# Performance work log

Hardware: AMD Instinct MI355X
Metric: run time of the kernel (lower is better)

The kernel has to match this reference:

```python
import jax, jax.numpy as jnp
import numpy as np

D_MODEL = 512; D_STATE = 64; D_CONV = 4; EXPAND = 1; HEADDIM = 128; NGROUPS = 2; CHUNK = 256
D_INNER = EXPAND * (D_MODEL // 2)          # 256
NHEADS = D_INNER // HEADDIM                 # 2
CONV_DIM = D_INNER + 2 * NGROUPS * D_STATE  # 512
D_IN_PROJ = CONV_DIM + NHEADS               # 514

def silu(x):
    return x * jax.nn.sigmoid(x)

def conv1x1(x, w, b):
    # x: (b,c,h,w), w: (o,c)
    return jnp.einsum('bchw,oc->bohw', x, w) + b[None, :, None, None]

def dwconv3x3(x, w, b):
    # depthwise 3x3, SAME padding; w: (c,1,3,3)
    c = x.shape[1]
    y = jax.lax.conv_general_dilated(x, w, (1, 1), 'SAME', feature_group_count=c,
                                     dimension_numbers=('NCHW', 'OIHW', 'NCHW'))
    return y + b[None, :, None, None]

def causal_dwconv1d(x, w, b):
    # x: (b,L,c); w: (c,k). Torch pads k-1 both sides then slices [:L] -> causal left pad.
    k = w.shape[1]
    xp = jnp.pad(x, ((0, 0), (k - 1, 0), (0, 0))).transpose(0, 2, 1)  # (b,c,L+k-1)
    y = jax.lax.conv_general_dilated(xp, w[:, None, :], (1,), 'VALID',
                                     feature_group_count=w.shape[0],
                                     dimension_numbers=('NCH', 'OIH', 'NCH'))
    return y.transpose(0, 2, 1) + b

def axis_attn(x, qw, qb, fw, fb, axis):
    # DualAxisAggAttn single-axis step
    qkv = conv1x1(x, qw, qb)
    c = x.shape[1]
    q, k, v = qkv[:, :1], qkv[:, 1:1 + c], qkv[:, 1 + c:]
    dim = -1 if axis == 'W' else -2
    scores = jax.nn.softmax(q, axis=dim)
    ctx = jnp.sum(k * scores, axis=dim, keepdims=True)
    out = x + jax.nn.sigmoid(v) * ctx
    return conv1x1(out, fw, fb)

def segsum(x):
    # x: (...,T) -> (...,T,T) lower-triangular segment sums, -inf above diagonal
    T = x.shape[-1]
    cs = jnp.cumsum(x, -1)
    d = cs[..., :, None] - cs[..., None, :]
    mask = jnp.tril(jnp.ones((T, T), bool))
    return jnp.where(mask, d, -jnp.inf)

def ssd(X, A, B, C, chunk):
    # Mamba2 SSD chunked scan. X: (b,l,h,p) = x*dt; A: (b,l,h) = dt*A_head; B,C: (b,l,h,n)
    b, l, h, p = X.shape; n = B.shape[-1]; c = l // chunk
    X = X.reshape(b, c, chunk, h, p)
    B = B.reshape(b, c, chunk, h, n)
    C = C.reshape(b, c, chunk, h, n)
    A = A.reshape(b, c, chunk, h).transpose(0, 3, 1, 2)  # (b,h,c,L)
    Acs = jnp.cumsum(A, -1)
    L = jnp.exp(segsum(A))  # (b,h,c,L,L) intra-chunk decay
    Yd = jnp.einsum('bclhn,bcshn,bhcls,bcshp->bclhp', C, B, L, X)
    dec = jnp.exp(Acs[..., -1:] - Acs)
    st = jnp.einsum('bclhn,bhcl,bclhp->bchpn', B, dec, X)  # chunk end-states
    st = jnp.concatenate([jnp.zeros_like(st[:, :1]), st], 1)
    dchunk = jnp.exp(segsum(jnp.pad(Acs[..., -1], ((0, 0), (0, 0), (1, 0)))))
    st = jnp.einsum('bhzc,bchpn->bzhpn', dchunk, st)[:, :-1]  # states entering each chunk
    Yo = jnp.einsum('bclhn,bchpn,bhcl->bclhp', C, st, jnp.exp(Acs))
    return (Yd + Yo).reshape(b, l, h, p)

def setup_inputs() -> dict:
    key = jax.random.key(0)
    ks = jax.random.split(key, 12)
    s = 0.02
    p = {}
    p['u'] = jax.random.normal(ks[0], (8, D_MODEL, 64, 64), jnp.float32)
    p['sc_w1'] = jax.random.normal(ks[1], (D_MODEL, D_MODEL)) * s
    p['sc_b1'] = jnp.zeros((D_MODEL,))
    p['sc_wdw'] = jax.random.normal(ks[2], (D_MODEL, 1, 3, 3)) * s
    p['sc_bdw'] = jnp.zeros((D_MODEL,))
    p['sc_w2'] = jax.random.normal(ks[3], (D_INNER, D_MODEL)) * s
    p['sc_b2'] = jnp.zeros((D_INNER,))
    p['mc_w'] = jax.random.normal(ks[4], (D_INNER, D_MODEL)) * s
    p['mc_b'] = jnp.zeros((D_INNER,))
    p['qkvW_w'] = jax.random.normal(ks[5], (1 + 2 * D_INNER, D_INNER)) * s
    p['qkvW_b'] = jnp.zeros((1 + 2 * D_INNER,))
    p['qkvH_w'] = jax.random.normal(ks[6], (1 + 2 * D_INNER, D_INNER)) * s
    p['qkvH_b'] = jnp.zeros((1 + 2 * D_INNER,))
    p['fuseW_w'] = jax.random.normal(ks[7], (D_INNER, D_INNER)) * s
    p['fuseW_b'] = jnp.zeros((D_INNER,))
    p['fuseH_w'] = jax.random.normal(ks[8], (D_INNER, D_INNER)) * s
    p['fuseH_b'] = jnp.zeros((D_INNER,))
    p['in_proj_w'] = jax.random.normal(ks[9], (D_IN_PROJ, D_INNER)) * s
    p['conv1d_w'] = jax.random.normal(ks[10], (CONV_DIM, D_CONV)) * s
    p['conv1d_b'] = jnp.zeros((CONV_DIM,))
    dt = np.exp(np.linspace(np.log(1e-3), np.log(0.1), NHEADS))
    p['dt_bias'] = jnp.asarray(dt + np.log(-np.expm1(-dt)), jnp.float32)
    p['A_log'] = jnp.asarray(np.log(np.linspace(1.0, 16.0, NHEADS)), jnp.float32)
    p['D'] = jnp.ones((NHEADS,))
    p['norm_w'] = jnp.ones((D_INNER,))
    p['outp_w'] = jax.random.normal(ks[11], (D_MODEL, 2 * D_INNER)) * s
    p['outp_b'] = jnp.zeros((D_MODEL,))
    return p

def reference(u, sc_w1, sc_b1, sc_wdw, sc_bdw, sc_w2, sc_b2, mc_w, mc_b,
              qkvW_w, qkvW_b, qkvH_w, qkvH_b, fuseW_w, fuseW_b, fuseH_w, fuseH_b,
              in_proj_w, conv1d_w, conv1d_b, dt_bias, A_log, D, norm_w, outp_w, outp_b):
    b, _, H, W = u.shape
    # short_conv branch (light_ConvBlock: 1x1 -> dw3x3 -> 1x1, all SiLU; BN folded into bias)
    z = silu(conv1x1(u, sc_w1, sc_b1))
    z = silu(dwconv3x3(z, sc_wdw, sc_bdw))
    z = silu(conv1x1(z, sc_w2, sc_b2))
    # main branch
    x = silu(conv1x1(u, mc_w, mc_b))
    x = axis_attn(x, qkvW_w, qkvW_b, fuseW_w, fuseW_b, 'W')
    x = axis_attn(x, qkvH_w, qkvH_b, fuseH_w, fuseH_b, 'H')
    seqlen = H * W
    u2 = x.transpose(0, 2, 3, 1).reshape(b, seqlen, D_INNER)  # b (h w) c
    xbcdt = u2 @ in_proj_w.T  # (b,l,d_in_proj)
    xBC = xbcdt[..., :CONV_DIM]
    dt = jax.nn.softplus(xbcdt[..., CONV_DIM:] + dt_bias)  # (b,l,h)
    A = -jnp.exp(A_log)  # (h,)
    xBC = silu(causal_dwconv1d(xBC, conv1d_w, conv1d_b))
    xs = xBC[..., :D_INNER]
    Bs = xBC[..., D_INNER:D_INNER + NGROUPS * D_STATE].reshape(b, seqlen, NGROUPS, D_STATE)
    Cs = xBC[..., D_INNER + NGROUPS * D_STATE:].reshape(b, seqlen, NGROUPS, D_STATE)
    Xh = xs.reshape(b, seqlen, NHEADS, HEADDIM)
    rep = NHEADS // NGROUPS
    Bh = jnp.repeat(Bs, rep, axis=2)
    Ch = jnp.repeat(Cs, rep, axis=2)
    y = ssd(Xh * dt[..., None], dt * A[None, None, :], Bh, Ch, CHUNK)
    y = y + Xh * D[None, None, :, None]  # D skip connection
    y = y.reshape(b, seqlen, D_INNER)
    # RMSNormGated with z=None -> plain RMSNorm
    y = y * jax.lax.rsqrt(jnp.mean(y * y, -1, keepdims=True) + 1e-5) * norm_w
    y = y.reshape(b, H, W, D_INNER).transpose(0, 3, 1, 2)
    y = jnp.concatenate([z, y], axis=1)
    return conv1x1(y, outp_w, outp_b)
```

## Files before the change

kernel.cpp:

```cpp
#include <hip/hip_runtime.h>
#include <hip/hip_bf16.h>
#include <cstddef>
#include <cstdint>

#define PTOT 32768
#define HWSZ 4096

typedef __attribute__((ext_vector_type(8))) short bf16x8;
typedef __attribute__((ext_vector_type(4))) short s16x4;
typedef __attribute__((ext_vector_type(4))) float f32x4;

__device__ __forceinline__ float sigf(float x){ return 1.f/(1.f+__expf(-x)); }
__device__ __forceinline__ float siluf(float x){ return x*sigf(x); }
__device__ __forceinline__ short f2b(float x){
  __hip_bfloat16 h = __float2bfloat16(x);
  return *reinterpret_cast<short*>(&h);
}
__device__ __forceinline__ float b2f(short s){
  unsigned u = ((unsigned)(unsigned short)s) << 16;
  return __uint_as_float(u);
}

__device__ __forceinline__ void gload16(const void* g, void* l){
  __builtin_amdgcn_global_load_lds(
      (const __attribute__((address_space(1))) unsigned int*)g,
      (__attribute__((address_space(3))) unsigned int*)l, 16, 0, 0);
}

__global__ __launch_bounds__(256) void k_cvtw(
    const float* __restrict__ s0, const float* __restrict__ s1, const float* __restrict__ s2,
    const float* __restrict__ s3, const float* __restrict__ s4,
    short* __restrict__ dst){
  int idx = blockIdx.x*256 + threadIdx.x;
  const float* s; int off;
  if      (idx <  262144){ s=s0; off=idx; }
  else if (idx <  393216){ s=s1; off=idx- 262144; }
  else if (idx <  524288){ s=s2; off=idx- 393216; }
  else if (idx <  655616){ s=s3; off=idx- 524288; }
  else if (idx <  917760){ s=s4; off=idx- 655616; }
  else return;
  dst[idx] = f2b(s[off]);
}

__global__ __launch_bounds__(256) void k_wcomp(
    const float* __restrict__ qkvHw, const float* __restrict__ fuWw,
    const float* __restrict__ fuWb,  const float* __restrict__ qkvHb,
    const float* __restrict__ inpw,  const float* __restrict__ fuHw,
    const float* __restrict__ fuHb,
    const float* __restrict__ scb1,  const float* __restrict__ mcb,
    short* __restrict__ wcomb, float* __restrict__ bcomb,
    short* __restrict__ wi2,   float* __restrict__ bi2,
    float* __restrict__ bzx)
{
  int blk = blockIdx.x;
  int tid = threadIdx.x;
  __shared__ float as[256];
  __shared__ float red[256];
  if (blk < 513){
    int i = blk;
    int r = (i==512) ? 0 : (i+1);
    as[tid]  = qkvHw[(size_t)r*256 + tid];
    red[tid] = as[tid] * fuWb[tid];
    __syncthreads();
    for (int off=128; off; off>>=1){ if (tid<off) red[tid]+=red[tid+off]; __syncthreads(); }
    float acc = 0.f;
    #pragma unroll 8
    for (int k=0;k<256;k++) acc += as[k]*fuWw[(size_t)k*256 + tid];
    wcomb[(size_t)(256+i)*256 + tid] = f2b(acc);
    if (tid==0) bcomb[256+i] = red[0] + qkvHb[r];
  } else if (blk < 769){
    int j = blk - 513;
    wcomb[(size_t)j*256 + tid] = f2b(fuWw[(size_t)j*256 + tid]);
    if (tid==0) bcomb[j] = fuWb[j];
  } else if (blk < 1283){
    int j = blk - 769;
    as[tid]  = inpw[(size_t)j*256 + tid];
    red[tid] = as[tid] * fuHb[tid];
    __syncthreads();
    for (int off=128; off; off>>=1){ if (tid<off) red[tid]+=red[tid+off]; __syncthreads(); }
    float acc = 0.f;
    #pragma unroll 8
    for (int k=0;k<256;k++) acc += as[k]*fuHw[(size_t)k*256 + tid];
    wi2[(size_t)j*256 + tid] = f2b(acc);
    if (tid==0) bi2[j] = red[0];
  } else {
    int j = (blk - 1283)*256 + tid;
    bzx[j] = (j < 512) ? scb1[j] : mcb[j-512];
  }
}

__global__ __launch_bounds__(256) void k_transpose(const float* __restrict__ in, short* __restrict__ out){
  __shared__ float tile[64][33];
  int b = blockIdx.z;
  int c0 = blockIdx.y * 64;
  int s0 = blockIdx.x * 32;
  int tx = threadIdx.x, ty = threadIdx.y;
  const float* ip = in + ((size_t)b*512 + c0)*HWSZ + s0;
  for (int i = ty; i < 64; i += 8) tile[i][tx] = ip[(size_t)i*HWSZ + tx];
  __syncthreads();
  for (int i = ty; i < 32; i += 8){
    unsigned lo = (unsigned)(unsigned short)f2b(tile[2*tx][i]);
    unsigned hi = (unsigned)(unsigned short)f2b(tile[2*tx+1][i]);
    unsigned pk = lo | (hi<<16);
    *reinterpret_cast<unsigned*>(&out[((size_t)((b<<12) + s0 + i))*512 + c0 + 2*tx]) = pk;
  }
}

template<int ACT, int OUT_NCHW>
__global__ __launch_bounds__(256) void k_gemm(
    const short* __restrict__ A0, const short* __restrict__ A1,
    int kSplit, int lda0, int lda1,
    const short* __restrict__ Wt, const float* __restrict__ bias,
    void* __restrict__ Cpv, int N, int K, int ldc, int qkvPerm,
    short* __restrict__ Cp2, int nSplit2, int ldc2)
{
  __shared__ short Alds[3][128*32];
  __shared__ short Wlds[2][128*32];

  int tid = threadIdx.x;
  int lane = tid & 63;
  int wv = tid >> 6;
  int wr = wv >> 1, wc = wv & 1;
  int lr = lane & 15, lh = lane >> 4;
  int bm = blockIdx.x * 128;
  int bn = blockIdx.y * 128;

  int rl = lane >> 2;
  int kg = (lane & 3) << 3;

  int ar[2], wnr[2];
  #pragma unroll
  for (int j=0;j<2;j++){
    int r = wv*32 + j*16 + rl;
    ar[j] = bm + r;
    int n = bn + r; if (n > N-1) n = N-1;
    wnr[j] = qkvPerm ? ((n==512)?0:(n+1)) : n;
  }

  auto stage_a = [&](int buf, int t){
    int k0 = t << 5;
    #pragma unroll
    for (int j=0;j<2;j++){
      const short* asrc;
      if (k0 < kSplit) asrc = A0 + (size_t)ar[j]*lda0 + (k0 + kg);
      else             asrc = A1 + (size_t)ar[j]*lda1 + (k0 - kSplit + kg);
      gload16(asrc, &Alds[buf][(wv*32 + j*16)*32]);
    }
  };
  auto stage_w = [&](int buf, int t){
    int k0 = t << 5;
    #pragma unroll
    for (int j=0;j<2;j++){
      const short* bsrc = Wt + (size_t)wnr[j]*K + (k0 + kg);
      gload16(bsrc, &Wlds[buf][(wv*32 + j*16)*32]);
    }
  };

  f32x4 acc[4][4];
  #pragma unroll
  for (int i=0;i<4;i++)
    #pragma unroll
    for (int j=0;j<4;j++) acc[i][j] = (f32x4){0.f,0.f,0.f,0.f};

  int NT = K >> 5;
  stage_w(0, 0);
  __builtin_amdgcn_sched_barrier(0);
  stage_a(0, 0);
  __builtin_amdgcn_sched_barrier(0);
  stage_a(1, 1);
  for (int t=0; t<NT; t++){
    int ab = t % 3, wb = t & 1;
    if (t+1 < NT) asm volatile("s_waitcnt vmcnt(2)" ::: "memory");
    else          asm volatile("s_waitcnt vmcnt(0)" ::: "memory");
    __builtin_amdgcn_s_barrier();
    __builtin_amdgcn_sched_barrier(0);
    if (t+1 < NT) stage_w(wb^1, t+1);
    __builtin_amdgcn_sched_barrier(0);
    if (t+2 < NT) stage_a((t+2)%3, t+2);
    __builtin_amdgcn_sched_barrier(0);
    bf16x8 af[4], bfr[4];
    #pragma unroll
    for (int mi=0;mi<4;mi++)
      af[mi] = *reinterpret_cast<const bf16x8*>(&Alds[ab][(wr*64 + mi*16 + lr)*32 + lh*8]);
    #pragma unroll
    for (int ni=0;ni<4;ni++)
      bfr[ni] = *reinterpret_cast<const bf16x8*>(&Wlds[wb][(wc*64 + ni*16 + lr)*32 + lh*8]);
    #pragma unroll
    for (int mi=0;mi<4;mi++)
      #pragma unroll
      for (int ni=0;ni<4;ni++)
        acc[mi][ni] = __builtin_amdgcn_mfma_f32_16x16x32_bf16(af[mi], bfr[ni], acc[mi][ni], 0, 0, 0);
  }

  if (!OUT_NCHW){
    short* Cp = (short*)Cpv;
    #pragma unroll
    for (int mi=0;mi<4;mi++){
      int m = bm + wr*64 + mi*16 + lh*4;
      #pragma unroll
      for (int ni=0;ni<4;ni++){
        int n = bn + wc*64 + ni*16 + lr;
        if (n < N){
          int wn = qkvPerm ? ((n==512)?0:(n+1)) : n;
          float bb = bias ? bias[wn] : 0.f;
          #pragma unroll
          for (int r=0;r<4;r++){
            float v = acc[mi][ni][r] + bb;
            if (ACT==1) v = siluf(v);
            short sv = f2b(v);
            if (n < nSplit2) Cp[(size_t)(m+r)*ldc + n] = sv;
            else             Cp2[(size_t)(m+r)*ldc2 + (n - nSplit2)] = sv;
          }
        }
      }
    }
  } else {
    float* Cp = (float*)Cpv;
    float* Sep = ((float*)Alds) + wv*16*68;
    #pragma unroll
    for (int mi=0;mi<4;mi++){
      __syncthreads();
      #pragma unroll
      for (int ni=0;ni<4;ni++){
        int n = bn + wc*64 + ni*16 + lr;
        float bb = (bias && n < N) ? bias[n] : 0.f;
        #pragma unroll
        for (int r=0;r<4;r++){
          float v = acc[mi][ni][r] + bb;
          if (ACT==1) v = siluf(v);
          Sep[(lh*4+r)*68 + ni*16 + lr] = v;
        }
      }
      __syncthreads();
      int m = bm + wr*64 + mi*16 + lr;
      size_t mb = ((size_t)(m>>12)*ldc)*HWSZ + (m & 4095);
      #pragma unroll
      for (int g=0; g<16; g++){
        int nl = g*4 + lh;
        float v = Sep[lr*68 + nl];
        int nn = bn + wc*64 + nl;
        if (nn < N) Cp[mb + (size_t)nn*HWSZ] = v;
      }
    }
  }
}

__global__ __launch_bounds__(256) void k_dwconv3x3(const short* __restrict__ in,
    const float* __restrict__ w, const float* __restrict__ bias, short* __restrict__ out){
  int tid = threadIdx.x;
  int cq = tid & 127;
  int wi = tid >> 7;
  int bw = blockIdx.x;
  int b  = bw >> 5;
  int wc = ((bw & 31) << 1) | wi;
  int h0 = blockIdx.y << 4;
  int c  = cq << 2;

  float arr[36];
  {
    const float* wp = &w[c*9];
    #pragma unroll
    for (int t=0;t<9;t++){
      f32x4 v = *reinterpret_cast<const f32x4*>(wp + t*4);
      arr[t*4+0]=v[0]; arr[t*4+1]=v[1]; arr[t*4+2]=v[2]; arr[t*4+3]=v[3];
    }
  }
  f32x4 bias4 = *reinterpret_cast<const f32x4*>(&bias[c]);

  int pb = b << 12;
  auto ldrow = [&](int r, int dw)->f32x4 {
    int ww = wc + dw;
    if ((unsigned)r >= 64u || (unsigned)ww >= 64u) return (f32x4){0.f,0.f,0.f,0.f};
    s16x4 v = *reinterpret_cast<const s16x4*>(&in[((size_t)(pb + (r<<6) + ww) << 9) + c]);
    return (f32x4){b2f(v[0]), b2f(v[1]), b2f(v[2]), b2f(v[3])};
  };

  f32x4 a00,a01,a02,a10,a11,a12,a20,a21,a22;
  a00=ldrow(h0-1,-1); a01=ldrow(h0-1,0); a02=ldrow(h0-1,1);
  a10=ldrow(h0  ,-1); a11=ldrow(h0  ,0); a12=ldrow(h0  ,1);
  #pragma unroll
  for (int hh=0; hh<16; hh++){
    int h = h0 + hh;
    a20=ldrow(h+1,-1); a21=ldrow(h+1,0); a22=ldrow(h+1,1);
    s16x4 o;
    #pragma unroll
    for (int j=0;j<4;j++){
      float v = bias4[j];
      v = fmaf(a00[j], arr[j*9+0], v);
      v = fmaf(a01[j], arr[j*9+1], v);
      v = fmaf(a02[j], arr[j*9+2], v);
      v = fmaf(a10[j], arr[j*9+3], v);
      v = fmaf(a11[j], arr[j*9+4], v);
      v = fmaf(a12[j], arr[j*9+5], v);
      v = fmaf(a20[j], arr[j*9+6], v);
      v = fmaf(a21[j], arr[j*9+7], v);
      v = fmaf(a22[j], arr[j*9+8], v);
      o[j] = f2b(siluf(v));
    }
    *reinterpret_cast<s16x4*>(&out[((size_t)(pb + (h<<6) + wc) << 9) + c]) = o;
    a00=a10; a01=a11; a02=a12;
    a10=a20; a11=a21; a12=a22;
  }
}

__global__ __launch_bounds__(256) void k_attn(const short* __restrict__ x, int xld,
    const short* __restrict__ qkv, int qld, short* __restrict__ out, int axisH){
  int bl = blockIdx.x;
  int b = bl >> 6, line = bl & 63;
  __shared__ float es[64];
  __shared__ float qs[64];
  int tid = threadIdx.x;
  int pbase = b << 12;
  if (tid < 64){
    int p = axisH ? (pbase | (tid<<6) | line) : (pbase | (line<<6) | tid);
    qs[tid] = b2f(qkv[(size_t)p*qld + 512]);
  }
  __syncthreads();
  float mx = -1e30f;
  for (int t=0;t<64;t++) mx = fmaxf(mx, qs[t]);
  if (tid < 64) es[tid] = __expf(qs[tid]-mx);
  __syncthreads();
  float s = 0.f;
  for (int t=0;t<64;t++) s += es[t];
  float inv = 1.f/s;
  int c = tid;
  float ctx = 0.f;
  for (int t=0;t<64;t++){
    int p = axisH ? (pbase | (t<<6) | line) : (pbase | (line<<6) | t);
    ctx += es[t]*b2f(qkv[(size_t)p*qld + c]);
  }
  ctx *= inv;
  for (int t=0;t<64;t++){
    int p = axisH ? (pbase | (t<<6) | line) : (pbase | (line<<6) | t);
    float vv = b2f(qkv[(size_t)p*qld + 256 + c]);
    float xv = b2f(x[(size_t)p*xld + c]);
    out[(size_t)p*256 + c] = f2b(xv + sigf(vv)*ctx);
  }
}

__global__ __launch_bounds__(256) void k_dt(const short* __restrict__ xbcdt,
    const float* __restrict__ dt_bias, float* __restrict__ dtb){
  int idx = blockIdx.x*256 + threadIdx.x;
  if (idx >= PTOT*2) return;
  int p = idx >> 1, h = idx & 1;
  float xv = b2f(xbcdt[(size_t)p*520 + 512 + h]) + dt_bias[h];
  float sp = (xv > 20.f) ? xv : log1pf(__expf(xv));
  dtb[idx] = sp;
}

__global__ __launch_bounds__(256) void k_conv1d(const short* __restrict__ xbcdt,
    const float* __restrict__ w, const float* __restrict__ bias, short* __restrict__ xBC){
  int tid = threadIdx.x;
  int cq = tid & 127;
  int c  = cq << 2;
  int half = tid >> 7;
  int bs = blockIdx.x;
  int b  = bs >> 7;
  int t0 = ((((bs & 127) << 1) | half) << 4);

  float wk[16];
  {
    const float* wp = &w[c*4];
    #pragma unroll
    for (int t=0;t<4;t++){
      f32x4 v = *reinterpret_cast<const f32x4*>(wp + t*4);
      wk[t*4+0]=v[0]; wk[t*4+1]=v[1]; wk[t*4+2]=v[2]; wk[t*4+3]=v[3];
    }
  }
  f32x4 bias4 = *reinterpret_cast<const f32x4*>(&bias[c]);

  int pb = b << 12;
  auto ld = [&](int t)->f32x4 {
    if (t < 0) return (f32x4){0.f,0.f,0.f,0.f};
    s16x4 v = *reinterpret_cast<const s16x4*>(&xbcdt[(size_t)(pb + t)*520 + c]);
    return (f32x4){b2f(v[0]), b2f(v[1]), b2f(v[2]), b2f(v[3])};
  };

  f32x4 x0,x1,x2,x3;
  x0 = ld(t0-3); x1 = ld(t0-2); x2 = ld(t0-1);
  #pragma unroll
  for (int tt=0; tt<16; tt++){
    int t = t0 + tt;
    x3 = ld(t);
    s16x4 o;
    #pragma unroll
    for (int j=0;j<4;j++){
      float v = bias4[j];
      v = fmaf(x0[j], wk[j*4+0], v);
      v = fmaf(x1[j], wk[j*4+1], v);
      v = fmaf(x2[j], wk[j*4+2], v);
      v = fmaf(x3[j], wk[j*4+3], v);
      o[j] = f2b(siluf(v));
    }
    *reinterpret_cast<s16x4*>(&xBC[((size_t)(pb + t) << 9) + c]) = o;
    x0=x1; x1=x2; x2=x3;
  }
}

__global__ __launch_bounds__(256) void k_ssd_states(
  const short* __restrict__ xBC, const float* __restrict__ dtb, const float* __restrict__ A_log,
  float* __restrict__ states, float* __restrict__ AcsG, float* __restrict__ AtotG)
{
  int ci = blockIdx.x, h = blockIdx.y, b = blockIdx.z;
  int tid = threadIdx.x;
  __shared__ float sa[256], sb[256];
  __shared__ float Bs[64][65];
  __shared__ float Xs[64][136];
  int base = (b<<12) | (ci<<8);
  float Ah = -__expf(A_log[h]);
  sa[tid] = dtb[(size_t)(base + tid)*2 + h] * Ah;
  __syncthreads();
  float* src = sa; float* dst = sb;
  for (int off=1; off<256; off<<=1){
    float v = src[tid];
    if (tid >= off) v += src[tid - off];
    dst[tid] = v;
    __syncthreads();
    float* tswap = src; src = dst; dst = tswap;
  }
  float acs = src[tid];
  float atot = src[255];
  AcsG[((size_t)((b*2+h)*16 + ci))*256 + tid] = acs;
  if (tid == 0) AtotG[(b*2+h)*16 + ci] = atot;

  int tn = tid >> 4;
  int tp = tid & 15;
  float acc[4][8];
  #pragma unroll
  for (int i=0;i<4;i++)
    #pragma unroll
    for (int j=0;j<8;j++) acc[i][j]=0.f;

  for (int t0=0; t0<256; t0+=64){
    __syncthreads();
    for (int e = tid; e < 64*64; e += 256){
      int t = e >> 6, n = e & 63;
      float d = __expf(atot - src[t0 + t]);
      Bs[t][n] = b2f(xBC[(size_t)(base + t0 + t)*512 + 256 + (h<<6) + n]) * d;
    }
    for (int e = tid; e < 64*128; e += 256){
      int t = e >> 7, pp = e & 127;
      Xs[t][pp] = b2f(xBC[(size_t)(base + t0 + t)*512 + (h<<7) + pp]) * dtb[(size_t)(base + t0 + t)*2 + h];
    }
    __syncthreads();
    for (int t=0;t<64;t++){
      float bv[4], xv[8];
      #pragma unroll
      for (int i=0;i<4;i++) bv[i]=Bs[t][tn*4+i];
      #pragma unroll
      for (int j=0;j<8;j++) xv[j]=Xs[t][tp*8+j];
      #pragma unroll
      for (int i=0;i<4;i++)
        #pragma unroll
        for (int j=0;j<8;j++) acc[i][j] = fmaf(bv[i], xv[j], acc[i][j]);
    }
  }
  float* stp = states + (((size_t)(b*16+ci)*2 + h) << 13);
  #pragma unroll
  for (int i=0;i<4;i++){
    float4 s0 = {acc[i][0], acc[i][1], acc[i][2], acc[i][3]};
    float4 s1 = {acc[i][4], acc[i][5], acc[i][6], acc[i][7]};
    float* pdst = &stp[(tn*4+i)*128 + tp*8];
    *reinterpret_cast<float4*>(pdst)   = s0;
    *reinterpret_cast<float4*>(pdst+4) = s1;
  }
}

__global__ __launch_bounds__(256) void k_ssd_scan(const float* __restrict__ states,
    const float* __restrict__ AtotG, float* __restrict__ R){
  int bh = blockIdx.x;
  int b = bh >> 1, h = bh & 1;
  int tid = threadIdx.x;
  float r[32];
  #pragma unroll
  for (int j=0;j<32;j++) r[j]=0.f;
  for (int ci=0; ci<16; ci++){
    size_t off = (((size_t)(b*16+ci)*2) + h) << 13;
    #pragma unroll
    for (int j=0;j<32;j++) R[off + tid + (j<<8)] = r[j];
    if (ci < 15){
      float sc = __expf(AtotG[bh*16 + ci]);
      #pragma unroll
      for (int j=0;j<32;j++) r[j] = fmaf(sc, r[j], states[off + tid + (j<<8)]);
    }
  }
}

__global__ __launch_bounds__(256) void k_ssd_y(
  const short* __restrict__ xBC, const float* __restrict__ dtb,
  const float* __restrict__ AcsG, const float* __restrict__ R,
  const float* __restrict__ Dp, float* __restrict__ yraw)
{
  int bx = blockIdx.x;
  int ci = bx >> 2, lt = bx & 3;
  int h = blockIdx.y, b = blockIdx.z;
  int tid = threadIdx.x, lane = tid & 63, w = tid >> 6;
  int lg = lane >> 4, lr = lane & 15;
  int base = (b<<12) | (ci<<8);
  int l0 = lt << 6;

  __shared__ short Cbf[64*72];
  __shared__ short Bbf[64*72];
  __shared__ short Xt [128*76];
  __shared__ short Sbf[64*72];
  __shared__ float acs_l[64], acs_s[64], dt_s[64];

  const float* acsrow = AcsG + ((size_t)((b*2+h)*16 + ci))*256;

  {
    int row = tid >> 2, c0 = (tid & 3) << 4;
    const short* src = &xBC[(size_t)(base + l0 + row)*512 + 384 + (h<<6) + c0];
    *reinterpret_cast<bf16x8*>(&Cbf[row*72 + c0])     = *reinterpret_cast<const bf16x8*>(src);
    *reinterpret_cast<bf16x8*>(&Cbf[row*72 + c0 + 8]) = *reinterpret_cast<const bf16x8*>(src+8);
  }
  if (tid < 64) acs_l[tid] = acsrow[l0 + tid];

  f32x4 yacc[8];
  #pragma unroll
  for (int pf=0;pf<8;pf++) yacc[pf] = (f32x4){0.f,0.f,0.f,0.f};

  for (int s0 = 0; s0 <= l0; s0 += 64){
    __syncthreads();
    {
      int row = tid >> 2, c0 = (tid & 3) << 4;
      const short* src = &xBC[(size_t)(base + s0 + row)*512 + 256 + (h<<6) + c0];
      *reinterpret_cast<bf16x8*>(&Bbf[row*72 + c0])     = *reinterpret_cast<const bf16x8*>(src);
      *reinterpret_cast<bf16x8*>(&Bbf[row*72 + c0 + 8]) = *reinterpret_cast<const bf16x8*>(src+8);
    }
    {
      int s = tid >> 2;
      int p0 = (tid & 3) << 5;
      const short* src = &xBC[(size_t)(base + s0 + s)*512 + (h<<7) + p0];
      #pragma unroll
      for (int q=0;q<4;q++){
        bf16x8 v = *reinterpret_cast<const bf16x8*>(src + q*8);
        #pragma unroll
        for (int e=0;e<8;e++) Xt[(p0 + q*8 + e)*76 + s] = v[e];
      }
    }
    if (tid < 64){
      acs_s[tid] = acsrow[s0 + tid];
      dt_s[tid]  = dtb[(size_t)(base + s0 + tid)*2 + h];
    }
    __syncthreads();

    f32x4 sacc[4];
    #pragma unroll
    for (int f=0;f<4;f++) sacc[f] = (f32x4){0.f,0.f,0.f,0.f};
    bf16x8 ca0 = *reinterpret_cast<const bf16x8*>(&Cbf[(w*16+lr)*72 + lg*8]);
    bf16x8 ca1 = *reinterpret_cast<const bf16x8*>(&Cbf[(w*16+lr)*72 + 32 + lg*8]);
    #pragma unroll
    for (int f=0;f<4;f++){
      bf16x8 bb0 = *reinterpret_cast<const bf16x8*>(&Bbf[(f*16+lr)*72 + lg*8]);
      bf16x8 bb1 = *reinterpret_cast<const bf16x8*>(&Bbf[(f*16+lr)*72 + 32 + lg*8]);
      sacc[f] = __builtin_amdgcn_mfma_f32_16x16x32_bf16(ca0, bb0, sacc[f], 0, 0, 0);
      sacc[f] = __builtin_amdgcn_mfma_f32_16x16x32_bf16(ca1, bb1, sacc[f], 0, 0, 0);
    }
    #pragma unroll
    for (int f=0;f<4;f++){
      #pragma unroll
      for (int r=0;r<4;r++){
        int ll = w*16 + lg*4 + r;
        int ss = f*16 + lr;
        float v = 0.f;
        if (s0 + ss <= l0 + ll)
          v = sacc[f][r] * __expf(acs_l[ll] - acs_s[ss]) * dt_s[ss];
        Sbf[ll*72 + ss] = f2b(v);
      }
    }
    __syncthreads();

    bf16x8 sa0 = *reinterpret_cast<const bf16x8*>(&Sbf[(w*16+lr)*72 + lg*8]);
    bf16x8 sa1 = *reinterpret_cast<const bf16x8*>(&Sbf[(w*16+lr)*72 + 32 + lg*8]);
    #pragma unroll
    for (int pf=0;pf<8;pf++){
      bf16x8 x0 = *reinterpret_cast<const bf16x8*>(&Xt[(pf*16+lr)*76 + lg*8]);
      bf16x8 x1 = *reinterpret_cast<const bf16x8*>(&Xt[(pf*16+lr)*76 + 32 + lg*8]);
      yacc[pf] = __builtin_amdgcn_mfma_f32_16x16x32_bf16(sa0, x0, yacc[pf], 0, 0, 0);
      yacc[pf] = __builtin_amdgcn_mfma_f32_16x16x32_bf16(sa1, x1, yacc[pf], 0, 0, 0);
    }
  }

  __syncthreads();
  {
    size_t roff = (((size_t)(b*16+ci)*2) + h) << 13;
    int n = tid >> 2;
    const float* src = R + roff + (size_t)n*128;
    #pragma unroll
    for (int j=0;j<8;j++){
      int p = ((tid & 3) << 2) + (j << 4);
      float4 f = *reinterpret_cast<const float4*>(&src[p]);
      Xt[(p+0)*76 + n] = f2b(f.x);
      Xt[(p+1)*76 + n] = f2b(f.y);
      Xt[(p+2)*76 + n] = f2b(f.z);
      Xt[(p+3)*76 + n] = f2b(f.w);
    }
  }
  __syncthreads();
  f32x4 racc[8];
  #pragma unroll
  for (int pf=0;pf<8;pf++) racc[pf] = (f32x4){0.f,0.f,0.f,0.f};
  {
    bf16x8 ca0 = *reinterpret_cast<const bf16x8*>(&Cbf[(w*16+lr)*72 + lg*8]);
    bf16x8 ca1 = *reinterpret_cast<const bf16x8*>(&Cbf[(w*16+lr)*72 + 32 + lg*8]);
    #pragma unroll
    for (int pf=0;pf<8;pf++){
      bf16x8 x0 = *reinterpret_cast<const bf16x8*>(&Xt[(pf*16+lr)*76 + lg*8]);
      bf16x8 x1 = *reinterpret_cast<const bf16x8*>(&Xt[(pf*16+lr)*76 + 32 + lg*8]);
      racc[pf] = __builtin_amdgcn_mfma_f32_16x16x32_bf16(ca0, x0, racc[pf], 0, 0, 0);
      racc[pf] = __builtin_amdgcn_mfma_f32_16x16x32_bf16(ca1, x1, racc[pf], 0, 0, 0);
    }
  }

  float Dh = Dp[h];
  float el[4];
  #pragma unroll
  for (int r=0;r<4;r++) el[r] = __expf(acs_l[w*16 + lg*4 + r]);
  #pragma unroll
  for (int pf=0;pf<8;pf++){
    #pragma unroll
    for (int r=0;r<4;r++){
      int ll = w*16 + lg*4 + r;
      int p = pf*16 + lr;
      size_t pix = (size_t)(base + l0 + ll);
      float xraw = b2f(xBC[pix*512 + (h<<7) + p]);
      yraw[pix*256 + (h<<7) + p] = yacc[pf][r] + el[r]*racc[pf][r] + Dh*xraw;
    }
  }
}

__global__ __launch_bounds__(256) void k_rmsnorm(const float* __restrict__ yraw,
    const float* __restrict__ nw, short* __restrict__ ynorm){
  int p = blockIdx.x;
  int tid = threadIdx.x;
  float v = yraw[(size_t)p*256 + tid];
  float sq = v*v;
  for (int off=32; off; off>>=1) sq += __shfl_down(sq, off);
  __shared__ float wsum[4];
  if ((tid & 63) == 0) wsum[tid>>6] = sq;
  __syncthreads();
  float tot = wsum[0]+wsum[1]+wsum[2]+wsum[3];
  float scale = rsqrtf(tot*(1.f/256.f) + 1e-5f);
  ynorm[(size_t)p*256 + tid] = f2b(v*scale*nw[tid]);
}

extern "C" void kernel_launch(void* const* d_in, const int* in_sizes, int n_in,
                              void* d_out, int out_size, void* d_ws, size_t ws_size,
                              hipStream_t stream)
{
  (void)in_sizes; (void)n_in; (void)out_size; (void)ws_size;
  const float* u        = (const float*)d_in[0];
  const float* sc_w1    = (const float*)d_in[1];
  const float* sc_b1    = (const float*)d_in[2];
  const float* sc_wdw   = (const float*)d_in[3];
  const float* sc_bdw   = (const float*)d_in[4];
  const float* sc_w2    = (const float*)d_in[5];
  const float* sc_b2    = (const float*)d_in[6];
  const float* mc_w     = (const float*)d_in[7];
  const float* mc_b     = (const float*)d_in[8];
  const float* qkvW_w   = (const float*)d_in[9];
  const float* qkvW_b   = (const float*)d_in[10];
  const float* qkvH_w   = (const float*)d_in[11];
  const float* qkvH_b   = (const float*)d_in[12];
  const float* fuseW_w  = (const float*)d_in[13];
  const float* fuseW_b  = (const float*)d_in[14];
  const float* fuseH_w  = (const float*)d_in[15];
  const float* fuseH_b  = (const float*)d_in[16];
  const float* in_proj_w= (const float*)d_in[17];
  const float* conv1d_w = (const float*)d_in[18];
  const float* conv1d_b = (const float*)d_in[19];
  const float* dt_bias  = (const float*)d_in[20];
  const float* A_log    = (const float*)d_in[21];
  const float* Dp       = (const float*)d_in[22];
  const float* norm_w   = (const float*)d_in[23];
  const float* outp_w   = (const float*)d_in[24];
  const float* outp_b   = (const float*)d_in[25];

  char* wsb = (char*)d_ws;
  size_t off = 0;
  auto alloc = [&](size_t bytes){ void* p = wsb + off; off = (off + bytes + 255) & ~(size_t)255; return p; };
  short* wbf   = (short*)alloc((size_t)1246208*2);
  float* bcomb = (float*)alloc(769*4);
  float* bi2   = (float*)alloc(514*4);
  float* bzx   = (float*)alloc(768*4);
  short* slotB = (short*)alloc((size_t)PTOT*776*2);
  short* slotC = (short*)alloc((size_t)PTOT*512*2);
  short* slotZ = (short*)alloc((size_t)PTOT*256*2);
  short* slotE = (short*)alloc((size_t)PTOT*256*2);
  float* slotF = (float*)alloc((size_t)PTOT*256*4);
  float* slotS = (float*)alloc((size_t)4460000*4);

  float* dtb     = slotS;
  float* AcsG    = slotS + 65536;
  float* AtotG   = slotS + 131072;
  float* statesB = slotS + 131328;
  float* Rb      = slotS + 131328 + 2097152;
  short* ynorm   = slotE;
  short* xwh     = (short*)slotF;

  short* w_zx   = wbf + 0;
  short* w_sc2  = wbf + 393216;
  short* w_qkvW = wbf + 524288;
  short* w_outp = wbf + 655616;
  short* wcomb  = wbf + 917760;
  short* wi2    = wbf + 1114624;

  short* u_pm = (short*)d_out;
  float* out  = (float*)d_out;

  const int BIG = 1<<30;

  k_cvtw<<<3585, 256, 0, stream>>>(sc_w1, mc_w, sc_w2, qkvW_w, outp_w, wbf);
  k_wcomp<<<1286, 256, 0, stream>>>(qkvH_w, fuseW_w, fuseW_b, qkvH_b, in_proj_w, fuseH_w, fuseH_b,
                                    sc_b1, mc_b, wcomb, bcomb, wi2, bi2, bzx);
  k_transpose<<<dim3(128,8,8), dim3(32,8), 0, stream>>>(u, u_pm);

  k_gemm<1,0><<<dim3(256,6), 256, 0, stream>>>(u_pm, u_pm, BIG, 512, 512, w_zx, bzx,
                                               slotB, 768, 512, 512, 0, slotE, 512, 256);
  k_dwconv3x3<<<dim3(256,4), 256, 0, stream>>>(slotB, sc_wdw, sc_bdw, slotC);
  k_gemm<1,0><<<dim3(256,2), 256, 0, stream>>>(slotC, slotC, BIG, 512, 512, w_sc2, sc_b2,
                                               slotZ, 256, 512, 256, 0, nullptr, BIG, 0);

  k_gemm<0,0><<<dim3(256,5), 256, 0, stream>>>(slotE, slotE, BIG, 256, 256, w_qkvW, qkvW_b,
                                               slotB, 513, 256, 520, 1, nullptr, BIG, 0);
  k_attn<<<512, 256, 0, stream>>>(slotE, 256, slotB, 520, xwh, 0);
  k_gemm<0,0><<<dim3(256,7), 256, 0, stream>>>(xwh, xwh, BIG, 256, 256, wcomb, bcomb,
                                               slotB, 769, 256, 776, 0, nullptr, BIG, 0);
  k_attn<<<512, 256, 0, stream>>>(slotB, 776, slotB + 256, 776, xwh, 1);
  k_gemm<0,0><<<dim3(256,5), 256, 0, stream>>>(xwh, xwh, BIG, 256, 256, wi2, bi2,
                                               slotB, 514, 256, 520, 0, nullptr, BIG, 0);
  k_dt<<<256, 256, 0, stream>>>(slotB, dt_bias, dtb);
  k_conv1d<<<1024, 256, 0, stream>>>(slotB, conv1d_w, conv1d_b, slotC);

  k_ssd_states<<<dim3(16,2,8), 256, 0, stream>>>(slotC, dtb, A_log, statesB, AcsG, AtotG);
  k_ssd_scan<<<16, 256, 0, stream>>>(statesB, AtotG, Rb);
  k_ssd_y<<<dim3(64,2,8), 256, 0, stream>>>(slotC, dtb, AcsG, Rb, Dp, slotF);

  k_rmsnorm<<<32768, 256, 0, stream>>>(slotF, norm_w, ynorm);

  k_gemm<0,1><<<dim3(256,4), 256, 0, stream>>>(slotZ, ynorm, 256, 256, 256, w_outp, outp_b,
                                               out, 512, 512, 512, 0, nullptr, BIG, 0);
}
```

Before: 477.3 us.

## Load GEMM weights directly to registers and single-buffer A tile in LDS

Rewrites the k_gemm main loop to drop the triple-buffered A and double-buffered W LDS pipeline. Weight fragments are now read straight from global memory into registers, and only a single A tile goes through LDS, guarded by two barriers per K step. Launch bounds request 4 blocks per CU, and the NCHW epilogue gets its own shared staging array. The aim is to cut LDS footprint and raise occupancy, at the cost of losing prefetch overlap and doing uncoalesced weight loads on every K step.

New measurement: 516.6 us. +8.2%, slower.

```diff
diff --git a/kernel.cpp b/kernel.cpp
--- a/kernel.cpp
+++ b/kernel.cpp
@@ -107,15 +107,14 @@
 }
 
 template<int ACT, int OUT_NCHW>
-__global__ __launch_bounds__(256) void k_gemm(
+__global__ __launch_bounds__(256, 4) void k_gemm(
     const short* __restrict__ A0, const short* __restrict__ A1,
     int kSplit, int lda0, int lda1,
     const short* __restrict__ Wt, const float* __restrict__ bias,
     void* __restrict__ Cpv, int N, int K, int ldc, int qkvPerm,
     short* __restrict__ Cp2, int nSplit2, int ldc2)
 {
-  __shared__ short Alds[3][128*32];
-  __shared__ short Wlds[2][128*32];
+  __shared__ short Alds[128*32];
 
   int tid = threadIdx.x;
   int lane = tid & 63;
@@ -128,33 +127,22 @@
   int rl = lane >> 2;
   int kg = (lane & 3) << 3;
 
-  int ar[2], wnr[2];
+  const short* aB0[2];
+  const short* aB1[2];
   #pragma unroll
   for (int j=0;j<2;j++){
-    int r = wv*32 + j*16 + rl;
-    ar[j] = bm + r;
-    int n = bn + r; if (n > N-1) n = N-1;
-    wnr[j] = qkvPerm ? ((n==512)?0:(n+1)) : n;
-  }
-
-  auto stage_a = [&](int buf, int t){
-    int k0 = t << 5;
-    #pragma unroll
-    for (int j=0;j<2;j++){
-      const short* asrc;
-      if (k0 < kSplit) asrc = A0 + (size_t)ar[j]*lda0 + (k0 + kg);
-      else             asrc = A1 + (size_t)ar[j]*lda1 + (k0 - kSplit + kg);
-      gload16(asrc, &Alds[buf][(wv*32 + j*16)*32]);
-    }
-  };
-  auto stage_w = [&](int buf, int t){
-    int k0 = t << 5;
-    #pragma unroll
-    for (int j=0;j<2;j++){
-      const short* bsrc = Wt + (size_t)wnr[j]*K + (k0 + kg);
-      gload16(bsrc, &Wlds[buf][(wv*32 + j*16)*32]);
-    }
-  };
+    int m = bm + wv*32 + j*16 + rl;
+    aB0[j] = A0 + (size_t)m*lda0 + kg;
+    aB1[j] = A1 + (size_t)m*lda1 + kg;
+  }
+  const short* wB[4];
+  #pragma unroll
+  for (int ni=0;ni<4;ni++){
+    int n = bn + wc*64 + ni*16 + lr;
+    if (n > N-1) n = N-1;
+    int wn = qkvPerm ? ((n==512)?0:(n+1)) : n;
+    wB[ni] = Wt + (size_t)wn*K + lh*8;
+  }
 
   f32x4 acc[4][4];
   #pragma unroll
@@ -162,34 +150,30 @@
     #pragma unroll
     for (int j=0;j<4;j++) acc[i][j] = (f32x4){0.f,0.f,0.f,0.f};
 
-  int NT = K >> 5;
-  stage_w(0, 0);
-  __builtin_amdgcn_sched_barrier(0);
-  stage_a(0, 0);
-  __builtin_amdgcn_sched_barrier(0);
-  stage_a(1, 1);
-  for (int t=0; t<NT; t++){
-    int ab = t % 3, wb = t & 1;
-    if (t+1 < NT) asm volatile("s_waitcnt vmcnt(2)" ::: "memory");
-    else          asm volatile("s_waitcnt vmcnt(0)" ::: "memory");
-    __builtin_amdgcn_s_barrier();
-    __builtin_amdgcn_sched_barrier(0);
-    if (t+1 < NT) stage_w(wb^1, t+1);
-    __builtin_amdgcn_sched_barrier(0);
-    if (t+2 < NT) stage_a((t+2)%3, t+2);
-    __builtin_amdgcn_sched_barrier(0);
-    bf16x8 af[4], bfr[4];
+  for (int k0 = 0; k0 < K; k0 += 32){
+    bf16x8 bfr[4];
+    #pragma unroll
+    for (int ni=0;ni<4;ni++)
+      bfr[ni] = *reinterpret_cast<const bf16x8*>(wB[ni] + k0);
+    {
+      const short* s0;
+      const short* s1;
+      if (k0 < kSplit){ s0 = aB0[0] + k0; s1 = aB0[1] + k0; }
+      else            { s0 = aB1[0] + (k0 - kSplit); s1 = aB1[1] + (k0 - kSplit); }
+      gload16(s0, &Alds[(wv*32)*32]);
+      gload16(s1, &Alds[(wv*32 + 16)*32]);
+    }
+    __syncthreads();
+    bf16x8 af[4];
     #pragma unroll
     for (int mi=0;mi<4;mi++)
-      af[mi] = *reinterpret_cast<const bf16x8*>(&Alds[ab][(wr*64 + mi*16 + lr)*32 + lh*8]);
-    #pragma unroll
-    for (int ni=0;ni<4;ni++)
-      bfr[ni] = *reinterpret_cast<const bf16x8*>(&Wlds[wb][(wc*64 + ni*16 + lr)*32 + lh*8]);
+      af[mi] = *reinterpret_cast<const bf16x8*>(&Alds[(wr*64 + mi*16 + lr)*32 + lh*8]);
     #pragma unroll
     for (int mi=0;mi<4;mi++)
       #pragma unroll
       for (int ni=0;ni<4;ni++)
         acc[mi][ni] = __builtin_amdgcn_mfma_f32_16x16x32_bf16(af[mi], bfr[ni], acc[mi][ni], 0, 0, 0);
+    __syncthreads();
   }
 
   if (!OUT_NCHW){
@@ -216,7 +200,8 @@
     }
   } else {
     float* Cp = (float*)Cpv;
-    float* Sep = ((float*)Alds) + wv*16*68;
+    __shared__ float S[4][16][68];
+    float* Sep = &S[wv][0][0];
     #pragma unroll
     for (int mi=0;mi<4;mi++){
       __syncthreads();
```
